# Performance work log

Measured on AMD Instinct MI355X. Metric: run time of the kernel, lower is better.

The kernel has to match this reference:

```python
import jax, jax.numpy as jnp
import numpy as np

B = 64          # graphs per batch
N = 1500        # nodes per graph (equal sizes -> vectorized sortpool)
NT = B * N      # total nodes
DEG = 16        # avg in-degree
E_PER = N * DEG # edges per graph
F_IN = 128
K = 30          # sortpool k
LATENT = [32, 32, 32, 1]  # total 97
TOTAL_LAT = sum(LATENT)
OUT_DIM = 128


def setup_inputs() -> dict:
    key = jax.random.key(0)
    ks = jax.random.split(key, 16)
    node_feat = jax.random.normal(ks[0], (NT, F_IN), dtype=jnp.float32)
    # edges constrained within each graph (block-diagonal adjacency)
    offs = (jnp.arange(B, dtype=jnp.int32) * N)[:, None]
    edge_src = (jax.random.randint(ks[1], (B, E_PER), 0, N, dtype=jnp.int32) + offs).reshape(-1)
    edge_dst = (jax.random.randint(ks[2], (B, E_PER), 0, N, dtype=jnp.int32) + offs).reshape(-1)

    def lin(k, fan_in, shape):
        return jax.random.normal(k, shape, dtype=jnp.float32) * (1.0 / np.sqrt(fan_in))

    inp = dict(node_feat=node_feat, edge_src=edge_src, edge_dst=edge_dst)
    dims = [F_IN] + LATENT
    for i in range(4):
        inp[f'W{i+1}'] = lin(ks[3 + i], dims[i], (dims[i], dims[i + 1]))
        inp[f'b{i+1}'] = jnp.zeros((dims[i + 1],), jnp.float32)
    inp['conv1_w'] = lin(ks[8], TOTAL_LAT, (16, TOTAL_LAT))   # Conv1d(1,16,97,stride=97)
    inp['conv1_b'] = jnp.zeros((16,), jnp.float32)
    inp['conv2_w'] = lin(ks[9], 16 * 5, (32, 16, 5))          # Conv1d(16,32,5)
    inp['conv2_b'] = jnp.zeros((32,), jnp.float32)
    inp['out_w'] = lin(ks[10], 352, (352, OUT_DIM))
    inp['out_b'] = jnp.zeros((OUT_DIM,), jnp.float32)
    return inp


def reference(node_feat, edge_src, edge_dst, W1, b1, W2, b2, W3, b3, W4, b4,
              conv1_w, conv1_b, conv2_w, conv2_b, out_w, out_b):
    # node degrees (+1 for self loop), from in-edges
    deg = jax.ops.segment_sum(jnp.ones_like(edge_dst, jnp.float32), edge_dst, num_segments=NT)
    node_degs = (deg + 1.0)[:, None]

    # 4 graph-conv layers: (A @ h + h) -> Linear -> /deg -> tanh, concat features
    h = node_feat
    layers = []
    for W, b in ((W1, b1), (W2, b2), (W3, b3), (W4, b4)):
        agg = jax.ops.segment_sum(h[edge_src], edge_dst, num_segments=NT) + h
        h = jnp.tanh((agg @ W + b) / node_degs)
        layers.append(h)
    feat = jnp.concatenate(layers, axis=1)  # [NT, 97]

    # sortpooling: top-k nodes per graph by the last channel
    sort_ch = feat[:, -1].reshape(B, N)
    _, idx = jax.lax.top_k(sort_ch, K)                    # [B, K]
    gidx = (idx + (jnp.arange(B, dtype=idx.dtype) * N)[:, None]).reshape(-1)
    pooled = feat[gidx].reshape(B, K, TOTAL_LAT)          # [B, K, 97]

    # Conv1d(1,16,97,stride=97) over flattened [B,1,K*97] == per-slot linear
    c1 = jax.nn.relu(jnp.einsum('bkd,od->bok', pooled, conv1_w) + conv1_b[None, :, None])  # [B,16,K]
    mp = c1.reshape(B, 16, K // 2, 2).max(axis=-1)        # MaxPool1d(2,2) -> [B,16,15]
    c2 = jax.lax.conv_general_dilated(mp, conv2_w, (1,), 'VALID',
                                      dimension_numbers=('NCH', 'OIH', 'NCH'))
    c2 = jax.nn.relu(c2 + conv2_b[None, :, None])         # [B,32,11]
    dense = c2.reshape(B, -1)                             # [B,352]
    return jax.nn.relu(dense @ out_w + out_b)             # relu(relu(x)) == relu(x)
```

## Files before the change

kernel.cpp:

```cpp
#include <hip/hip_runtime.h>

constexpr int B = 64, N = 1500, NT = B * N;
constexpr int E_PER = 24000, E_TOT = B * E_PER;
constexpr int E_PAD = 28512;
constexpr int F_INN = 128, K = 30, TOT = 97;
constexpr int NB_G = 47;
constexpr int GEMM_TILES = NT / 128;
constexpr int GEMM_BLKS = (GEMM_TILES + 3) / 4;

__global__ __launch_bounds__(1024) void prep(const int* __restrict__ src, const int* __restrict__ dst,
                                             int* __restrict__ csr, int* __restrict__ rowst,
                                             int* __restrict__ degi, float* __restrict__ degf,
                                             float* __restrict__ tA, float* __restrict__ tB,
                                             float* __restrict__ t4,
                                             const float* __restrict__ nf, const float* __restrict__ W1) {
    __shared__ union {
        struct { int hist[N]; int csr_l[E_PAD]; int wsum[4]; } c;
        struct { float hs[4][32][128]; float Ws[4][32][32]; } g;
    } u;
    int bid = blockIdx.x, t = threadIdx.x;

    if (bid < B) {
        int g = bid;
        int gbase = g * N;
        const int* dstg = dst + (size_t)g * E_PER;
        const int* srcg = src + (size_t)g * E_PER;

        if (g == 0) {
            if (t < 32) tA[(size_t)NT * 32 + t] = 0.f;
            else if (t < 64) tB[(size_t)NT * 32 + (t - 32)] = 0.f;
            else if (t == 64) t4[NT] = 0.f;
        }

        for (int i = t; i < N; i += 1024) u.c.hist[i] = 0;
        for (int i = t; i < E_PAD; i += 1024) u.c.csr_l[i] = NT;
        __syncthreads();
        for (int e = t; e < E_PER; e += 1024)
            atomicAdd(&u.c.hist[dstg[e] - gbase], 1);
        __syncthreads();

        int local[6];
        int sum = 0, x = 0;
        if (t < 256) {
#pragma unroll
            for (int i = 0; i < 6; ++i) {
                int v = t * 6 + i;
                int d = (v < N) ? u.c.hist[v] : 0;
                local[i] = d;
                sum += (d + 3) & ~3;
            }
            x = sum;
            int lane = t & 63;
#pragma unroll
            for (int m = 1; m < 64; m <<= 1) {
                int y = __shfl_up(x, m, 64);
                if (lane >= m) x += y;
            }
            if (lane == 63) u.c.wsum[t >> 6] = x;
        }
        __syncthreads();
        if (t < 256) {
            int woff = 0;
            int wv = t >> 6;
            for (int w = 0; w < wv; ++w) woff += u.c.wsum[w];
            int run = x - sum + woff;
#pragma unroll
            for (int i = 0; i < 6; ++i) {
                int v = t * 6 + i;
                if (v < N) {
                    rowst[gbase + v] = g * E_PAD + run;
                    degi[gbase + v] = local[i];
                    degf[gbase + v] = (float)(local[i] + 1);
                    u.c.hist[v] = run;
                    run += (local[i] + 3) & ~3;
                }
            }
        }
        __syncthreads();
        for (int e = t; e < E_PER; e += 1024) {
            int d = dstg[e] - gbase;
            int pos = atomicAdd(&u.c.hist[d], 1);
            u.c.csr_l[pos] = srcg[e];
        }
        __syncthreads();
        for (int i = t; i < E_PAD; i += 1024)
            csr[(size_t)g * E_PAD + i] = u.c.csr_l[i];
    } else {
        int sub = t >> 8, tid = t & 255;
        int tile = (bid - B) * 4 + sub;
        bool valid = tile < GEMM_TILES;
        int wv = tid >> 6, lane = tid & 63;
        int v0 = tile * 128;
        int og = wv * 8;
        float acc[2][8];
#pragma unroll
        for (int i = 0; i < 2; ++i)
#pragma unroll
            for (int j = 0; j < 8; ++j) acc[i][j] = 0.f;

        for (int kc = 0; kc < F_INN; kc += 32) {
            __syncthreads();
            if (valid) {
                int n = tid >> 1, kh = (tid & 1) * 16;
                const float* hp = nf + (size_t)(v0 + n) * F_INN + kc + kh;
                const float4* hp4 = reinterpret_cast<const float4*>(hp);
                float4 a = hp4[0], b = hp4[1], c = hp4[2], d = hp4[3];
                float (*hs)[128] = u.g.hs[sub];
                hs[kh + 0][n] = a.x;  hs[kh + 1][n] = a.y;  hs[kh + 2][n] = a.z;  hs[kh + 3][n] = a.w;
                hs[kh + 4][n] = b.x;  hs[kh + 5][n] = b.y;  hs[kh + 6][n] = b.z;  hs[kh + 7][n] = b.w;
                hs[kh + 8][n] = c.x;  hs[kh + 9][n] = c.y;  hs[kh + 10][n] = c.z; hs[kh + 11][n] = c.w;
                hs[kh + 12][n] = d.x; hs[kh + 13][n] = d.y; hs[kh + 14][n] = d.z; hs[kh + 15][n] = d.w;
                int r = tid >> 3, c4 = (tid & 7) * 4;
                float4 w = *reinterpret_cast<const float4*>(W1 + (size_t)(kc + r) * 32 + c4);
                *reinterpret_cast<float4*>(&u.g.Ws[sub][r][c4]) = w;
            }
            __syncthreads();
            if (valid) {
#pragma unroll
                for (int k = 0; k < 32; ++k) {
                    float2 hv = *reinterpret_cast<const float2*>(&u.g.hs[sub][k][2 * lane]);
                    float4 w0 = *reinterpret_cast<const float4*>(&u.g.Ws[sub][k][og]);
                    float4 w1 = *reinterpret_cast<const float4*>(&u.g.Ws[sub][k][og + 4]);
                    acc[0][0] += hv.x * w0.x; acc[0][1] += hv.x * w0.y; acc[0][2] += hv.x * w0.z; acc[0][3] += hv.x * w0.w;
                    acc[0][4] += hv.x * w1.x; acc[0][5] += hv.x * w1.y; acc[0][6] += hv.x * w1.z; acc[0][7] += hv.x * w1.w;
                    acc[1][0] += hv.y * w0.x; acc[1][1] += hv.y * w0.y; acc[1][2] += hv.y * w0.z; acc[1][3] += hv.y * w0.w;
                    acc[1][4] += hv.y * w1.x; acc[1][5] += hv.y * w1.y; acc[1][6] += hv.y * w1.z; acc[1][7] += hv.y * w1.w;
                }
            }
        }
        if (valid) {
#pragma unroll
            for (int i = 0; i < 2; ++i) {
                float* op = tA + (size_t)(v0 + 2 * lane + i) * 32 + og;
                float4 r0 = {acc[i][0], acc[i][1], acc[i][2], acc[i][3]};
                float4 r1 = {acc[i][4], acc[i][5], acc[i][6], acc[i][7]};
                reinterpret_cast<float4*>(op)[0] = r0;
                reinterpret_cast<float4*>(op)[1] = r1;
            }
        }
    }
}

template <int FUSE>
__global__ __launch_bounds__(256) void agg_f(const float* __restrict__ t,
                                             const int* __restrict__ csr, const int* __restrict__ rowst,
                                             const int* __restrict__ degi, const float* __restrict__ degf,
                                             const float* __restrict__ bias, const float* __restrict__ Wn,
                                             float* __restrict__ hout, float* __restrict__ tn) {
    __shared__ float Ws[1024];
    __shared__ float outs[32][32];
    if (FUSE == 32) {
        for (int i = threadIdx.x; i < 1024; i += 256) Ws[i] = Wn[i];
    }
    int bid = blockIdx.x;
    int xcd = bid & 7, j = bid >> 3;
    int g = xcd + 8 * (j / NB_G);
    int nb = j % NB_G;
    int nl = threadIdx.x >> 3;
    int f4 = threadIdx.x & 7;
    int vl = nb * 32 + nl;
    bool valid = vl < N;
    int v = g * N + vl;
    const float4* t4v = reinterpret_cast<const float4*>(t);
    float4 out = {0.f, 0.f, 0.f, 0.f};
    if (valid) {
        float4 acc = t4v[(unsigned)(v * 8 + f4)];
        int e0 = rowst[v];
        int dc = degi[v];
        int pc = (dc + 3) & ~3;
        float4 s1 = {0.f, 0.f, 0.f, 0.f}, s2 = {0.f, 0.f, 0.f, 0.f};
        for (int e = 0; e < pc; e += 4) {
            int4 s4 = *reinterpret_cast<const int4*>(csr + e0 + e);
            float4 x0 = t4v[(unsigned)(s4.x * 8 + f4)];
            float4 x1 = t4v[(unsigned)(s4.y * 8 + f4)];
            float4 x2 = t4v[(unsigned)(s4.z * 8 + f4)];
            float4 x3 = t4v[(unsigned)(s4.w * 8 + f4)];
            s1.x += x0.x + x1.x; s1.y += x0.y + x1.y; s1.z += x0.z + x1.z; s1.w += x0.w + x1.w;
            s2.x += x2.x + x3.x; s2.y += x2.y + x3.y; s2.z += x2.z + x3.z; s2.w += x2.w + x3.w;
        }
        acc.x += s1.x + s2.x; acc.y += s1.y + s2.y; acc.z += s1.z + s2.z; acc.w += s1.w + s2.w;
        float4 bv = *reinterpret_cast<const float4*>(bias + f4 * 4);
        float inv = 1.0f / degf[v];
        out.x = tanhf((acc.x + bv.x) * inv);
        out.y = tanhf((acc.y + bv.y) * inv);
        out.z = tanhf((acc.z + bv.z) * inv);
        out.w = tanhf((acc.w + bv.w) * inv);
        reinterpret_cast<float4*>(hout)[(unsigned)(v * 8 + f4)] = out;
    }
    if (FUSE == 32) {
        *reinterpret_cast<float4*>(&outs[nl][f4 * 4]) = out;
        __syncthreads();
        if (valid) {
            float4 s = {0.f, 0.f, 0.f, 0.f};
#pragma unroll
            for (int ff = 0; ff < 32; ++ff) {
                float h = outs[nl][ff];
                float4 wr = *reinterpret_cast<const float4*>(&Ws[ff * 32 + f4 * 4]);
                s.x += h * wr.x; s.y += h * wr.y; s.z += h * wr.z; s.w += h * wr.w;
            }
            reinterpret_cast<float4*>(tn)[(unsigned)(v * 8 + f4)] = s;
        }
    } else if (valid) {
        float4 w4 = *reinterpret_cast<const float4*>(Wn + f4 * 4);
        float p = out.x * w4.x + out.y * w4.y + out.z * w4.z + out.w * w4.w;
        p += __shfl_xor(p, 4, 64);
        p += __shfl_xor(p, 2, 64);
        p += __shfl_xor(p, 1, 64);
        if (f4 == 0) tn[v] = p;
    }
}

__global__ __launch_bounds__(512) void sort_head(const float* __restrict__ hc1, const float* __restrict__ hc2,
                                                 const float* __restrict__ hc3, const float* __restrict__ t4,
                                                 const int* __restrict__ csr, const int* __restrict__ rowst,
                                                 const int* __restrict__ degi, const float* __restrict__ degf,
                                                 const float* __restrict__ b4,
                                                 const float* __restrict__ c1w, const float* __restrict__ c1b,
                                                 const float* __restrict__ c2w, const float* __restrict__ c2b,
                                                 const float* __restrict__ ow, const float* __restrict__ ob,
                                                 float* __restrict__ out) {
    __shared__ float ts[N + 1];
    __shared__ unsigned int svals[N];
    __shared__ float fvals[N];
    __shared__ int hist[2048];
    __shared__ int canA[N], canB[N];
    __shared__ int winners[32];
    __shared__ int wsum[8];
    __shared__ int st_need, st_ncand, st_tb, st_cab, st_nwin;
    __shared__ int topk_s[K];
    __shared__ float pooled[K][TOT];
    __shared__ float c1[16][K];
    __shared__ float mp[16][16];
    __shared__ float dense[352];
    __shared__ float part[4][128];

    int g = blockIdx.x, t = threadIdx.x;
    int gbase = g * N;
    int lane = t & 63, w = t >> 6;

    for (int v = t; v < N; v += 512) ts[v] = t4[gbase + v];
    if (t == 0) ts[N] = 0.f;
    if (t == 1) { st_need = K; st_nwin = 0; }
    __syncthreads();
    {
        float b4v = b4[0];
        for (int v = t; v < N; v += 512) {
            int gv = gbase + v;
            int e0 = rowst[gv], dc = degi[gv];
            int pc = (dc + 3) & ~3;
            float a0 = 0.f, a1 = 0.f, a2 = 0.f, a3 = 0.f;
            for (int e = 0; e < pc; e += 4) {
                int4 s4 = *reinterpret_cast<const int4*>(csr + e0 + e);
                unsigned l0 = min((unsigned)(s4.x - gbase), (unsigned)N);
                unsigned l1 = min((unsigned)(s4.y - gbase), (unsigned)N);
                unsigned l2 = min((unsigned)(s4.z - gbase), (unsigned)N);
                unsigned l3 = min((unsigned)(s4.w - gbase), (unsigned)N);
                a0 += ts[l0];
                a1 += ts[l1];
                a2 += ts[l2];
                a3 += ts[l3];
            }
            float h = tanhf((ts[v] + (a0 + a1) + (a2 + a3) + b4v) / degf[gv]);
            fvals[v] = h;
            unsigned int b = __float_as_uint(h);
            svals[v] = (b & 0x80000000u) ? ~b : (b | 0x80000000u);
        }
    }
    __syncthreads();

    auto mkkey = [&](int idx) {
        return ((unsigned long long)svals[idx] << 31) | (unsigned int)(0x7FFFFFFF - idx);
    };

    const int SHIFTS[6] = {52, 41, 30, 19, 8, 0};
    int curN = N;
    int src = 0;
    for (int pass = 0; pass < 6; ++pass) {
        int shift = SHIFTS[pass];
        int mask = (pass == 5) ? 0xFF : 0x7FF;
        for (int i = t; i < 2048; i += 512) hist[i] = 0;
        if (t == 0) st_ncand = 0;
        __syncthreads();
        for (int i = t; i < curN; i += 512) {
            int idx = (src == 0) ? i : (src == 1 ? canA[i] : canB[i]);
            int d = (int)((mkkey(idx) >> shift) & mask);
            atomicAdd(&hist[d], 1);
        }
        __syncthreads();
        int need = st_need;
        int c[4];
        int s = 0;
#pragma unroll
        for (int u = 0; u < 4; ++u) { c[u] = hist[2047 - (4 * t + u)]; s += c[u]; }
        int x = s;
#pragma unroll
        for (int m = 1; m < 64; m <<= 1) {
            int y = __shfl_up(x, m, 64);
            if (lane >= m) x += y;
        }
        if (lane == 63) wsum[w] = x;
        __syncthreads();
        int woff = 0;
        for (int ww = 0; ww < w; ++ww) woff += wsum[ww];
        int A = woff + x - s;
#pragma unroll
        for (int u = 0; u < 4; ++u) {
            if (A < need && need <= A + c[u]) { st_tb = 2047 - (4 * t + u); st_cab = A; }
            A += c[u];
        }
        __syncthreads();
        int tb = st_tb, cab = st_cab;
        int* dst = (src == 1) ? canB : canA;
        for (int i = t; i < curN; i += 512) {
            int idx = (src == 0) ? i : (src == 1 ? canA[i] : canB[i]);
            int d = (int)((mkkey(idx) >> shift) & mask);
            if (d > tb) {
                int p = atomicAdd(&st_nwin, 1);
                winners[p] = idx;
            } else if (d == tb) {
                int p = atomicAdd(&st_ncand, 1);
                dst[p] = idx;
            }
        }
        __syncthreads();
        int ncand = st_ncand;
        need -= cab;
        if (t == 0) st_need = need;
        if (ncand == need) {
            int base = st_nwin;
            for (int i = t; i < ncand; i += 512) winners[base + i] = dst[i];
            __syncthreads();
            break;
        }
        curN = ncand;
        src = (src == 1) ? 2 : 1;
        __syncthreads();
    }

    if (t < 64) {
        unsigned long long key = (t < K) ? mkkey(winners[t]) : 0ull;
        unsigned long long kk = ~key;
#pragma unroll
        for (int k = 2; k <= 64; k <<= 1) {
#pragma unroll
            for (int j = k >> 1; j > 0; j >>= 1) {
                unsigned long long o = __shfl_xor(kk, j, 64);
                bool keepMin = ((t & j) == 0) == ((t & k) == 0);
                kk = keepMin ? (kk < o ? kk : o) : (kk > o ? kk : o);
            }
        }
        key = ~kk;
        if (t < K) topk_s[t] = 0x7FFFFFFF - (int)(unsigned int)(key & 0x7FFFFFFFu);
    }
    __syncthreads();

    for (int i = t; i < K * TOT; i += 512) {
        int k = i / TOT, d = i % TOT;
        int vloc = topk_s[k];
        int gi = gbase + vloc;
        float val = (d < 32) ? hc1[(size_t)gi * 32 + d]
                  : (d < 64) ? hc2[(size_t)gi * 32 + d - 32]
                  : (d < 96) ? hc3[(size_t)gi * 32 + d - 64]
                             : fvals[vloc];
        pooled[k][d] = val;
    }
    __syncthreads();
    for (int i = t; i < 16 * K; i += 512) {
        int o = i / K, k = i % K;
        float s = c1b[o];
        for (int d = 0; d < TOT; ++d) s += pooled[k][d] * c1w[o * TOT + d];
        c1[o][k] = fmaxf(s, 0.f);
    }
    __syncthreads();
    for (int i = t; i < 16 * 15; i += 512) {
        int o = i / 15, p = i % 15;
        mp[o][p] = fmaxf(c1[o][2 * p], c1[o][2 * p + 1]);
    }
    __syncthreads();
    for (int i = t; i < 352; i += 512) {
        int o = i / 11, p = i % 11;
        float s = c2b[o];
#pragma unroll
        for (int ci = 0; ci < 16; ++ci)
#pragma unroll
            for (int tt = 0; tt < 5; ++tt)
                s += mp[ci][p + tt] * c2w[(o * 16 + ci) * 5 + tt];
        dense[i] = fmaxf(s, 0.f);
    }
    __syncthreads();
    {
        int o = t & 127, q = t >> 7;
        float s = 0.f;
        for (int m = q * 88; m < (q + 1) * 88; ++m) s += dense[m] * ow[m * 128 + o];
        part[q][o] = s;
    }
    __syncthreads();
    if (t < 128) {
        float s = (part[0][t] + part[1][t]) + (part[2][t] + part[3][t]) + ob[t];
        out[g * 128 + t] = fmaxf(s, 0.f);
    }
}

extern "C" void kernel_launch(void* const* d_in, const int* in_sizes, int n_in,
                              void* d_out, int out_size, void* d_ws, size_t ws_size,
                              hipStream_t stream) {
    const float* node_feat = (const float*)d_in[0];
    const int* esrc = (const int*)d_in[1];
    const int* edst = (const int*)d_in[2];
    const float* W1 = (const float*)d_in[3];
    const float* b1 = (const float*)d_in[4];
    const float* W2 = (const float*)d_in[5];
    const float* b2 = (const float*)d_in[6];
    const float* W3 = (const float*)d_in[7];
    const float* b3 = (const float*)d_in[8];
    const float* W4 = (const float*)d_in[9];
    const float* b4 = (const float*)d_in[10];
    const float* c1w = (const float*)d_in[11];
    const float* c1b = (const float*)d_in[12];
    const float* c2w = (const float*)d_in[13];
    const float* c2b = (const float*)d_in[14];
    const float* ow = (const float*)d_in[15];
    const float* ob = (const float*)d_in[16];

    char* ws = (char*)d_ws;
    size_t off = 0;
    auto alloc = [&](size_t bytes) {
        size_t r = off;
        off += (bytes + 255) & ~(size_t)255;
        return r;
    };
    int* deg_i = (int*)(ws + alloc((size_t)NT * 4));
    int* rowst = (int*)(ws + alloc((size_t)NT * 4));
    float* degf = (float*)(ws + alloc((size_t)NT * 4));
    int* csr = (int*)(ws + alloc((size_t)B * E_PAD * 4));
    float* tA = (float*)(ws + alloc((size_t)(NT + 1) * 32 * 4));
    float* tB = (float*)(ws + alloc((size_t)(NT + 1) * 32 * 4));
    float* hc1 = (float*)(ws + alloc((size_t)NT * 32 * 4));
    float* hc2 = (float*)(ws + alloc((size_t)NT * 32 * 4));
    float* hc3 = (float*)(ws + alloc((size_t)NT * 32 * 4));
    float* t4 = (float*)(ws + alloc((size_t)(NT + 1) * 4));

    prep<<<B + GEMM_BLKS, 1024, 0, stream>>>(esrc, edst, csr, rowst, deg_i, degf,
                                             tA, tB, t4, node_feat, W1);

    agg_f<32><<<8 * NB_G * 8, 256, 0, stream>>>(tA, csr, rowst, deg_i, degf, b1, W2, hc1, tB);
    agg_f<32><<<8 * NB_G * 8, 256, 0, stream>>>(tB, csr, rowst, deg_i, degf, b2, W3, hc2, tA);
    agg_f<1><<<8 * NB_G * 8, 256, 0, stream>>>(tA, csr, rowst, deg_i, degf, b3, W4, hc3, t4);

    sort_head<<<B, 512, 0, stream>>>(hc1, hc2, hc3, t4, csr, rowst, deg_i, degf, b4,
                                     c1w, c1b, c2w, c2b, ow, ob, (float*)d_out);
}
```

Before: 120.2 us.

## Store CSR as graph-local 16-bit indices padded with self-loops, unroll by eight

The CSR neighbour lists now hold 16-bit graph-local node indices instead of 32-bit global ones, and each row is padded to a multiple of eight. Padding slots reuse the node's own index, and the self term is scaled by (1 + deg - padded) so the extra entries cancel out. This removes the zero-sentinel row and the clamp logic, halves index traffic, and lets the aggregation loop issue eight gathers per iteration. The GEMM part of prep also shares a single W1 tile across its four sub-tiles. In exchange, padding to eight adds more redundant gathers per row and a larger padded buffer.

```diff
diff --git a/kernel.cpp b/kernel.cpp
--- a/kernel.cpp
+++ b/kernel.cpp
@@ -2,38 +2,31 @@
 
 constexpr int B = 64, N = 1500, NT = B * N;
 constexpr int E_PER = 24000, E_TOT = B * E_PER;
-constexpr int E_PAD = 28512;
+constexpr int E_PAD = 34560;
 constexpr int F_INN = 128, K = 30, TOT = 97;
 constexpr int NB_G = 47;
 constexpr int GEMM_TILES = NT / 128;
 constexpr int GEMM_BLKS = (GEMM_TILES + 3) / 4;
 
 __global__ __launch_bounds__(1024) void prep(const int* __restrict__ src, const int* __restrict__ dst,
-                                             int* __restrict__ csr, int* __restrict__ rowst,
+                                             ushort* __restrict__ csr, int* __restrict__ rowst,
                                              int* __restrict__ degi, float* __restrict__ degf,
-                                             float* __restrict__ tA, float* __restrict__ tB,
-                                             float* __restrict__ t4,
+                                             float* __restrict__ tA,
                                              const float* __restrict__ nf, const float* __restrict__ W1) {
     __shared__ union {
-        struct { int hist[N]; int csr_l[E_PAD]; int wsum[4]; } c;
-        struct { float hs[4][32][128]; float Ws[4][32][32]; } g;
+        struct { int hist[N]; uint csr_l32[E_PAD / 2]; int wsum[4]; } c;
+        struct { float hs[4][32][128]; float Ws[32][32]; } g;
     } u;
     int bid = blockIdx.x, t = threadIdx.x;
 
     if (bid < B) {
+        ushort* csr_l = (ushort*)u.c.csr_l32;
         int g = bid;
         int gbase = g * N;
         const int* dstg = dst + (size_t)g * E_PER;
         const int* srcg = src + (size_t)g * E_PER;
 
-        if (g == 0) {
-            if (t < 32) tA[(size_t)NT * 32 + t] = 0.f;
-            else if (t < 64) tB[(size_t)NT * 32 + (t - 32)] = 0.f;
-            else if (t == 64) t4[NT] = 0.f;
-        }
-
         for (int i = t; i < N; i += 1024) u.c.hist[i] = 0;
-        for (int i = t; i < E_PAD; i += 1024) u.c.csr_l[i] = NT;
         __syncthreads();
         for (int e = t; e < E_PER; e += 1024)
             atomicAdd(&u.c.hist[dstg[e] - gbase], 1);
@@ -47,7 +40,7 @@
                 int v = t * 6 + i;
                 int d = (v < N) ? u.c.hist[v] : 0;
                 local[i] = d;
-                sum += (d + 3) & ~3;
+                sum += (d + 7) & ~7;
             }
             x = sum;
             int lane = t & 63;
@@ -72,7 +65,7 @@
                     degi[gbase + v] = local[i];
                     degf[gbase + v] = (float)(local[i] + 1);
                     u.c.hist[v] = run;
-                    run += (local[i] + 3) & ~3;
+                    run += (local[i] + 7) & ~7;
                 }
             }
         }
@@ -80,11 +73,15 @@
         for (int e = t; e < E_PER; e += 1024) {
             int d = dstg[e] - gbase;
             int pos = atomicAdd(&u.c.hist[d], 1);
-            u.c.csr_l[pos] = srcg[e];
-        }
-        __syncthreads();
-        for (int i = t; i < E_PAD; i += 1024)
-            csr[(size_t)g * E_PAD + i] = u.c.csr_l[i];
+            csr_l[pos] = (ushort)(srcg[e] - gbase);
+        }
+        __syncthreads();
+        for (int v = t; v < N; v += 1024)
+            for (int s = u.c.hist[v]; s & 7; ++s) csr_l[s] = (ushort)v;
+        __syncthreads();
+        uint* cg = (uint*)(csr + (size_t)g * E_PAD);
+        for (int i = t; i < E_PAD / 2; i += 1024)
+            cg[i] = u.c.csr_l32[i];
     } else {
         int sub = t >> 8, tid = t & 255;
         int tile = (bid - B) * 4 + sub;
@@ -110,17 +107,19 @@
                 hs[kh + 4][n] = b.x;  hs[kh + 5][n] = b.y;  hs[kh + 6][n] = b.z;  hs[kh + 7][n] = b.w;
                 hs[kh + 8][n] = c.x;  hs[kh + 9][n] = c.y;  hs[kh + 10][n] = c.z; hs[kh + 11][n] = c.w;
                 hs[kh + 12][n] = d.x; hs[kh + 13][n] = d.y; hs[kh + 14][n] = d.z; hs[kh + 15][n] = d.w;
+            }
+            if (sub == 0) {
                 int r = tid >> 3, c4 = (tid & 7) * 4;
                 float4 w = *reinterpret_cast<const float4*>(W1 + (size_t)(kc + r) * 32 + c4);
-                *reinterpret_cast<float4*>(&u.g.Ws[sub][r][c4]) = w;
+                *reinterpret_cast<float4*>(&u.g.Ws[r][c4]) = w;
             }
             __syncthreads();
             if (valid) {
 #pragma unroll
                 for (int k = 0; k < 32; ++k) {
                     float2 hv = *reinterpret_cast<const float2*>(&u.g.hs[sub][k][2 * lane]);
-                    float4 w0 = *reinterpret_cast<const float4*>(&u.g.Ws[sub][k][og]);
-                    float4 w1 = *reinterpret_cast<const float4*>(&u.g.Ws[sub][k][og + 4]);
+                    float4 w0 = *reinterpret_cast<const float4*>(&u.g.Ws[k][og]);
+                    float4 w1 = *reinterpret_cast<const float4*>(&u.g.Ws[k][og + 4]);
                     acc[0][0] += hv.x * w0.x; acc[0][1] += hv.x * w0.y; acc[0][2] += hv.x * w0.z; acc[0][3] += hv.x * w0.w;
                     acc[0][4] += hv.x * w1.x; acc[0][5] += hv.x * w1.y; acc[0][6] += hv.x * w1.z; acc[0][7] += hv.x * w1.w;
                     acc[1][0] += hv.y * w0.x; acc[1][1] += hv.y * w0.y; acc[1][2] += hv.y * w0.z; acc[1][3] += hv.y * w0.w;
@@ -143,7 +142,7 @@
 
 template <int FUSE>
 __global__ __launch_bounds__(256) void agg_f(const float* __restrict__ t,
-                                             const int* __restrict__ csr, const int* __restrict__ rowst,
+                                             const ushort* __restrict__ csr, const int* __restrict__ rowst,
                                              const int* __restrict__ degi, const float* __restrict__ degf,
                                              const float* __restrict__ bias, const float* __restrict__ Wn,
                                              float* __restrict__ hout, float* __restrict__ tn) {
@@ -161,24 +160,38 @@
     int vl = nb * 32 + nl;
     bool valid = vl < N;
     int v = g * N + vl;
+    int gb8 = g * N * 8;
     const float4* t4v = reinterpret_cast<const float4*>(t);
     float4 out = {0.f, 0.f, 0.f, 0.f};
     if (valid) {
-        float4 acc = t4v[(unsigned)(v * 8 + f4)];
+        float4 tself = t4v[(unsigned)(v * 8 + f4)];
         int e0 = rowst[v];
         int dc = degi[v];
-        int pc = (dc + 3) & ~3;
+        int pc = (dc + 7) & ~7;
+        float scale = (float)(1 + dc - pc);
+        float4 acc = {scale * tself.x, scale * tself.y, scale * tself.z, scale * tself.w};
         float4 s1 = {0.f, 0.f, 0.f, 0.f}, s2 = {0.f, 0.f, 0.f, 0.f};
-        for (int e = 0; e < pc; e += 4) {
-            int4 s4 = *reinterpret_cast<const int4*>(csr + e0 + e);
-            float4 x0 = t4v[(unsigned)(s4.x * 8 + f4)];
-            float4 x1 = t4v[(unsigned)(s4.y * 8 + f4)];
-            float4 x2 = t4v[(unsigned)(s4.z * 8 + f4)];
-            float4 x3 = t4v[(unsigned)(s4.w * 8 + f4)];
+        float4 s3 = {0.f, 0.f, 0.f, 0.f}, s4v = {0.f, 0.f, 0.f, 0.f};
+        for (int e = 0; e < pc; e += 8) {
+            ushort4 ia = *reinterpret_cast<const ushort4*>(csr + e0 + e);
+            ushort4 ib = *reinterpret_cast<const ushort4*>(csr + e0 + e + 4);
+            float4 x0 = t4v[(unsigned)(gb8 + ia.x * 8 + f4)];
+            float4 x1 = t4v[(unsigned)(gb8 + ia.y * 8 + f4)];
+            float4 x2 = t4v[(unsigned)(gb8 + ia.z * 8 + f4)];
+            float4 x3 = t4v[(unsigned)(gb8 + ia.w * 8 + f4)];
+            float4 x4 = t4v[(unsigned)(gb8 + ib.x * 8 + f4)];
+            float4 x5 = t4v[(unsigned)(gb8 + ib.y * 8 + f4)];
+            float4 x6 = t4v[(unsigned)(gb8 + ib.z * 8 + f4)];
+            float4 x7 = t4v[(unsigned)(gb8 + ib.w * 8 + f4)];
             s1.x += x0.x + x1.x; s1.y += x0.y + x1.y; s1.z += x0.z + x1.z; s1.w += x0.w + x1.w;
             s2.x += x2.x + x3.x; s2.y += x2.y + x3.y; s2.z += x2.z + x3.z; s2.w += x2.w + x3.w;
-        }
-        acc.x += s1.x + s2.x; acc.y += s1.y + s2.y; acc.z += s1.z + s2.z; acc.w += s1.w + s2.w;
+            s3.x += x4.x + x5.x; s3.y += x4.y + x5.y; s3.z += x4.z + x5.z; s3.w += x4.w + x5.w;
+            s4v.x += x6.x + x7.x; s4v.y += x6.y + x7.y; s4v.z += x6.z + x7.z; s4v.w += x6.w + x7.w;
+        }
+        acc.x += (s1.x + s2.x) + (s3.x + s4v.x);
+        acc.y += (s1.y + s2.y) + (s3.y + s4v.y);
+        acc.z += (s1.z + s2.z) + (s3.z + s4v.z);
+        acc.w += (s1.w + s2.w) + (s3.w + s4v.w);
         float4 bv = *reinterpret_cast<const float4*>(bias + f4 * 4);
         float inv = 1.0f / degf[v];
         out.x = tanhf((acc.x + bv.x) * inv);
@@ -212,14 +225,14 @@
 
 __global__ __launch_bounds__(512) void sort_head(const float* __restrict__ hc1, const float* __restrict__ hc2,
                                                  const float* __restrict__ hc3, const float* __restrict__ t4,
-                                                 const int* __restrict__ csr, const int* __restrict__ rowst,
+                                                 const ushort* __restrict__ csr, const int* __restrict__ rowst,
                                                  const int* __restrict__ degi, const float* __restrict__ degf,
                                                  const float* __restrict__ b4,
                                                  const float* __restrict__ c1w, const float* __restrict__ c1b,
                                                  const float* __restrict__ c2w, const float* __restrict__ c2b,
                                                  const float* __restrict__ ow, const float* __restrict__ ob,
                                                  float* __restrict__ out) {
-    __shared__ float ts[N + 1];
+    __shared__ float ts[N];
     __shared__ unsigned int svals[N];
     __shared__ float fvals[N];
     __shared__ int hist[2048];
@@ -239,28 +252,24 @@
     int lane = t & 63, w = t >> 6;
 
     for (int v = t; v < N; v += 512) ts[v] = t4[gbase + v];
-    if (t == 0) ts[N] = 0.f;
-    if (t == 1) { st_need = K; st_nwin = 0; }
+    if (t == 0) { st_need = K; st_nwin = 0; }
     __syncthreads();
     {
         float b4v = b4[0];
         for (int v = t; v < N; v += 512) {
             int gv = gbase + v;
             int e0 = rowst[gv], dc = degi[gv];
-            int pc = (dc + 3) & ~3;
+            int pc = (dc + 7) & ~7;
+            float scale = (float)(1 + dc - pc);
             float a0 = 0.f, a1 = 0.f, a2 = 0.f, a3 = 0.f;
             for (int e = 0; e < pc; e += 4) {
-                int4 s4 = *reinterpret_cast<const int4*>(csr + e0 + e);
-                unsigned l0 = min((unsigned)(s4.x - gbase), (unsigned)N);
-                unsigned l1 = min((unsigned)(s4.y - gbase), (unsigned)N);
-                unsigned l2 = min((unsigned)(s4.z - gbase), (unsigned)N);
-                unsigned l3 = min((unsigned)(s4.w - gbase), (unsigned)N);
-                a0 += ts[l0];
-                a1 += ts[l1];
-                a2 += ts[l2];
-                a3 += ts[l3];
-            }
-            float h = tanhf((ts[v] + (a0 + a1) + (a2 + a3) + b4v) / degf[gv]);
+                ushort4 s4 = *reinterpret_cast<const ushort4*>(csr + e0 + e);
+                a0 += ts[s4.x];
+                a1 += ts[s4.y];
+                a2 += ts[s4.z];
+                a3 += ts[s4.w];
+            }
+            float h = tanhf((scale * ts[v] + (a0 + a1) + (a2 + a3) + b4v) / degf[gv]);
             fvals[v] = h;
             unsigned int b = __float_as_uint(h);
             svals[v] = (b & 0x80000000u) ? ~b : (b | 0x80000000u);
@@ -432,16 +441,16 @@
     int* deg_i = (int*)(ws + alloc((size_t)NT * 4));
     int* rowst = (int*)(ws + alloc((size_t)NT * 4));
     float* degf = (float*)(ws + alloc((size_t)NT * 4));
-    int* csr = (int*)(ws + alloc((size_t)B * E_PAD * 4));
-    float* tA = (float*)(ws + alloc((size_t)(NT + 1) * 32 * 4));
-    float* tB = (float*)(ws + alloc((size_t)(NT + 1) * 32 * 4));
+    ushort* csr = (ushort*)(ws + alloc((size_t)B * E_PAD * 2));
+    float* tA = (float*)(ws + alloc((size_t)NT * 32 * 4));
+    float* tB = (float*)(ws + alloc((size_t)NT * 32 * 4));
     float* hc1 = (float*)(ws + alloc((size_t)NT * 32 * 4));
     float* hc2 = (float*)(ws + alloc((size_t)NT * 32 * 4));
     float* hc3 = (float*)(ws + alloc((size_t)NT * 32 * 4));
-    float* t4 = (float*)(ws + alloc((size_t)(NT + 1) * 4));
+    float* t4 = (float*)(ws + alloc((size_t)NT * 4));
 
     prep<<<B + GEMM_BLKS, 1024, 0, stream>>>(esrc, edst, csr, rowst, deg_i, degf,
-                                             tA, tB, t4, node_feat, W1);
+                                             tA, node_feat, W1);
 
     agg_f<32><<<8 * NB_G * 8, 256, 0, stream>>>(tA, csr, rowst, deg_i, degf, b1, W2, hc1, tB);
     agg_f<32><<<8 * NB_G * 8, 256, 0, stream>>>(tB, csr, rowst, deg_i, degf, b2, W3, hc2, tA);
```

Result: faster. 117.2 us (-2.5%).
